# Kernel tuning notes

Measured on AMD Instinct MI355X. Metric: run time of the kernel, lower is better.

The kernel has to match this reference:

```python
import jax, jax.numpy as jnp
import numpy as np

N_CLUSTERS = 2048
MAX_ITER = 5


def setup_inputs() -> dict:
    key = jax.random.key(0)
    k1, k2 = jax.random.split(key)
    X = jax.random.normal(k1, (131072, 128), dtype=jnp.float32)
    init_centroids = jax.random.normal(k2, (N_CLUSTERS, 128), dtype=jnp.float32)
    return {"X": X, "init_centroids": init_centroids}


def _euc_sim(a, b):
    # 2 a.b^T - |a|^2 - |b|^2  (negative squared euclidean distance)
    return (2.0 * (a @ b.T)
            - jnp.sum(a * a, axis=1)[:, None]
            - jnp.sum(b * b, axis=1)[None, :])


def reference(X, init_centroids):
    K = init_centroids.shape[0]

    def step(centroids, _):
        sim = _euc_sim(X, centroids)              # [N, K]
        closest = jnp.argmax(sim, axis=-1)         # [N]
        sums = jax.ops.segment_sum(X, closest, num_segments=K)        # [K, d]
        counts = jax.ops.segment_sum(jnp.ones_like(closest, dtype=X.dtype),
                                     closest, num_segments=K)         # [K]
        # full-batch branch: c_grad = mask @ x / mask.sum(-1), NaN -> 0
        c_grad = jnp.where(counts[:, None] > 0, sums / jnp.maximum(counts, 1.0)[:, None], 0.0)
        # minibatch is None => lr = 1 => centroids <- c_grad
        return c_grad, closest

    centroids, closest_hist = jax.lax.scan(step, init_centroids, None, length=MAX_ITER)
    labels = closest_hist[-1]
    return centroids, labels
```

## Files before the change

### kernel.cpp

```cpp
#include <hip/hip_runtime.h>
#include <hip/hip_bf16.h>

#define NP 131072
#define D 128
#define KC 2048
#define ITERS 5
#define CG 8

#define TAU 0.03f
#define CNOFF 49152

#if defined(__has_builtin)
#if __has_builtin(__builtin_amdgcn_global_load_lds)
#define USE_GLL 1
#endif
#endif

typedef short bf16x8 __attribute__((ext_vector_type(8)));
typedef float f32x4 __attribute__((ext_vector_type(4)));

__device__ inline unsigned short f2bf(float x) {
    __hip_bfloat16 b = __float2bfloat16(x);
    return *reinterpret_cast<unsigned short*>(&b);
}
__device__ inline float bf2f(unsigned short u) {
    union { unsigned int i; float f; } c; c.i = ((unsigned int)u) << 16; return c.f;
}

__device__ inline size_t pslot(int k, int d, int hl) {
    int g = k >> 4, t15 = k & 15, ks = d >> 5, q = (d >> 3) & 3, e = d & 7;
    return ((size_t)((ks * 128 + g) * 2 + hl)) * 512 + (q * 16 + t15) * 8 + e;
}

#if USE_GLL
#define GLL16(srcp, dstp) __builtin_amdgcn_global_load_lds( \
    (const __attribute__((address_space(1))) unsigned int*)(srcp), \
    (__attribute__((address_space(3))) unsigned int*)(dstp), 16, 0, 0)
#define GLL4(srcp, dstp) __builtin_amdgcn_global_load_lds( \
    (const __attribute__((address_space(1))) unsigned int*)(srcp), \
    (__attribute__((address_space(3))) unsigned int*)(dstp), 4, 0, 0)
#else
#define GLL16(srcp, dstp) do { *(uint4*)((char*)(dstp) + lane * 16) = *(const uint4*)(srcp); } while (0)
#define GLL4(srcp, dstp)  do { *(unsigned int*)((char*)(dstp) + lane * 4) = *(const unsigned int*)(srcp); } while (0)
#endif

__global__ void init_kernel(const float* __restrict__ initC,
                            double* __restrict__ C64, double* __restrict__ CT64,
                            unsigned short* __restrict__ Pn) {
    int t = blockIdx.x * 256 + threadIdx.x;
    float v = initC[t];
    C64[t] = (double)v;
    CT64[(size_t)(t & 127) * KC + (t >> 7)] = (double)v;
    unsigned short h = f2bf(v);
    int k = t >> 7, d = t & 127;
    Pn[pslot(k, d, 0)] = h;
    Pn[pslot(k, d, 1)] = f2bf(v - bf2f(h));
}

__global__ void cnorm_kernel(const double* __restrict__ C64,
                             double* __restrict__ n64, float* __restrict__ n32,
                             int* __restrict__ counter) {
    int r = blockIdx.x * 4 + (threadIdx.x >> 6);
    int lane = threadIdx.x & 63;
    double a = C64[(size_t)r * D + lane * 2];
    double b = C64[(size_t)r * D + lane * 2 + 1];
    double s = a * a + b * b;
#pragma unroll
    for (int m = 1; m < 64; m <<= 1) s += __shfl_xor(s, m, 64);
    if (lane == 0) { n64[r] = s; n32[r] = (float)s; }
    if (blockIdx.x == 0 && threadIdx.x == 0) *counter = 0;
}

__global__ __launch_bounds__(256, 3)
void assign_kernel(const float* __restrict__ X,
                   const unsigned short* __restrict__ Pn,
                   const float* __restrict__ cnorm,
                   int* __restrict__ labels,
                   int* __restrict__ list,
                   int* __restrict__ counter) {
    __shared__ __align__(16) char lds[49664];

    const int tid = threadIdx.x;
    const int lane = tid & 63;
    const int wid = tid >> 6;
    const int wrow = wid >> 1;
    const int wcol = wid & 1;
    const int t15 = lane & 15;
    const int q = lane >> 4;
    const int pbase = blockIdx.x * 64;
    const char* PnB = (const char*)Pn;

#pragma unroll
    for (int i = 0; i < 8; i++) {
        int f = i * 256 + tid;
        int row = f >> 5, c4 = f & 31;
        float4 v = *(const float4*)&X[(size_t)(pbase + row) * D + c4 * 4];
        unsigned short h0 = f2bf(v.x), h1 = f2bf(v.y), h2 = f2bf(v.z), h3 = f2bf(v.w);
        unsigned short l0 = f2bf(v.x - bf2f(h0)), l1 = f2bf(v.y - bf2f(h1));
        unsigned short l2 = f2bf(v.z - bf2f(h2)), l3 = f2bf(v.w - bf2f(h3));
        uint2 ph = { (unsigned)h0 | ((unsigned)h1 << 16), (unsigned)h2 | ((unsigned)h3 << 16) };
        uint2 pl = { (unsigned)l0 | ((unsigned)l1 << 16), (unsigned)l2 | ((unsigned)l3 << 16) };
        int ad = (row * 256 + c4 * 8) ^ ((row & 7) << 4);
        *(uint2*)(lds + ad) = ph;
        *(uint2*)(lds + 16384 + ad) = pl;
    }
    __syncthreads();

    bf16x8 rah[2][4], ral[2][4];
#pragma unroll
    for (int rt = 0; rt < 2; rt++) {
        int row = wrow * 32 + rt * 16 + t15;
        int sw = (row & 7) << 4;
#pragma unroll
        for (int ks = 0; ks < 4; ks++) {
            int ad = (row * 256 + ks * 64 + q * 16) ^ sw;
            rah[rt][ks] = *(const bf16x8*)(lds + ad);
            ral[rt][ks] = *(const bf16x8*)(lds + 16384 + ad);
        }
    }
    __syncthreads();

    float b1[8], b2[8];
    int i1[8];
#pragma unroll
    for (int s = 0; s < 8; s++) { b1[s] = -INFINITY; b2[s] = -INFINITY; i1[s] = 0x7fffffff; }

#pragma unroll
    for (int i = 0; i < 4; i++) {
        int seg = wid * 4 + i;
        GLL16(PnB + seg * 1024 + lane * 16, lds + seg * 1024);
    }
#pragma unroll
    for (int i = 0; i < 4; i++) {
        int seg = wid * 4 + i;
        GLL16(PnB + (size_t)(1 * 128) * 2048 + seg * 1024 + lane * 16,
              lds + 16384 + seg * 1024);
    }

#define STEP(KS, VMSTR) do {                                                  \
        asm volatile("s_waitcnt vmcnt(" VMSTR ")" ::: "memory");              \
        __builtin_amdgcn_s_barrier();                                         \
        asm volatile("" ::: "memory");                                        \
        __builtin_amdgcn_sched_barrier(0);                                    \
        int t_ = ct * 4 + (KS);                                               \
        int s2_ = t_ + 2;                                                     \
        int s2c_ = (s2_ > 63) ? 63 : s2_;                                     \
        char* bstage_ = lds + (unsigned)(s2_ % 3) * 16384;                    \
        const char* nsrc_ = PnB + ((size_t)((s2c_ & 3) * 128 + (s2c_ >> 2) * 8)) * 2048; \
        _Pragma("unroll")                                                     \
        for (int i_ = 0; i_ < 4; i_++) {                                      \
            int seg_ = wid * 4 + i_;                                          \
            GLL16(nsrc_ + seg_ * 1024 + lane * 16, bstage_ + seg_ * 1024);    \
        }                                                                     \
        if ((KS) == 0) {                                                      \
            const float* cs_ = cnorm + ct * 128;                              \
            GLL4(cs_ + lane, lds + CNOFF);                                    \
            GLL4(cs_ + 64 + lane, lds + CNOFF + 256);                         \
        }                                                                     \
        const char* bcur_ = lds + (unsigned)(t_ % 3) * 16384;                 \
        __builtin_amdgcn_s_setprio(1);                                        \
        _Pragma("unroll")                                                     \
        for (int cj_ = 0; cj_ < 4; cj_++) {                                   \
            int gl_ = wcol * 4 + cj_;                                         \
            bf16x8 bh_ = *(const bf16x8*)(bcur_ + gl_ * 2048 + lane * 16);    \
            bf16x8 bl_ = *(const bf16x8*)(bcur_ + gl_ * 2048 + 1024 + lane * 16); \
            _Pragma("unroll")                                                 \
            for (int rt_ = 0; rt_ < 2; rt_++) {                               \
                acc[rt_][cj_] = __builtin_amdgcn_mfma_f32_16x16x32_bf16(rah[rt_][KS], bh_, acc[rt_][cj_], 0, 0, 0); \
                acc[rt_][cj_] = __builtin_amdgcn_mfma_f32_16x16x32_bf16(rah[rt_][KS], bl_, acc[rt_][cj_], 0, 0, 0); \
                acc[rt_][cj_] = __builtin_amdgcn_mfma_f32_16x16x32_bf16(ral[rt_][KS], bh_, acc[rt_][cj_], 0, 0, 0); \
            }                                                                 \
        }                                                                     \
        __builtin_amdgcn_s_setprio(0);                                        \
    } while (0)

    for (int ct = 0; ct < KC / 128; ct++) {
        f32x4 acc[2][4];
#pragma unroll
        for (int rt = 0; rt < 2; rt++)
#pragma unroll
            for (int cj = 0; cj < 4; cj++) acc[rt][cj] = (f32x4){0.f, 0.f, 0.f, 0.f};

        STEP(0, "4");
        STEP(1, "6");
        STEP(2, "6");
        STEP(3, "4");

        const float* cnL = (const float*)(lds + CNOFF);
#pragma unroll
        for (int cj = 0; cj < 4; cj++) {
            int col = ct * 128 + wcol * 64 + cj * 16 + t15;
            float cnv = cnL[wcol * 64 + cj * 16 + t15];
#pragma unroll
            for (int rt = 0; rt < 2; rt++)
#pragma unroll
                for (int rg = 0; rg < 4; rg++) {
                    int s = rt * 4 + rg;
                    float sv = __builtin_fmaf(2.0f, acc[rt][cj][rg], -cnv);
                    bool gt1 = sv > b1[s];
                    float mx2 = fmaxf(b2[s], sv);
                    b2[s] = gt1 ? b1[s] : mx2;
                    i1[s] = gt1 ? col : i1[s];
                    b1[s] = gt1 ? sv : b1[s];
                }
        }
    }
#undef STEP

#pragma unroll
    for (int s = 0; s < 8; s++) {
#pragma unroll
        for (int m = 1; m < 16; m <<= 1) {
            float ob1 = __shfl_xor(b1[s], m, 64);
            int   oi  = __shfl_xor(i1[s], m, 64);
            float ob2 = __shfl_xor(b2[s], m, 64);
            bool gt = ob1 > b1[s];
            bool eq = ob1 == b1[s];
            float nb2 = gt ? fmaxf(b1[s], ob2) : fmaxf(b2[s], ob1);
            nb2 = eq ? b1[s] : nb2;
            int ni = gt ? oi : i1[s];
            ni = (eq && oi < i1[s]) ? oi : ni;
            b1[s] = gt ? ob1 : b1[s];
            b2[s] = nb2;
            i1[s] = ni;
        }
    }

    __syncthreads();
    float* mb1 = (float*)lds;
    float* mb2 = ((float*)lds) + 128;
    int*   mi1 = (int*)(((float*)lds) + 256);
    if (t15 == 0) {
#pragma unroll
        for (int rt = 0; rt < 2; rt++)
#pragma unroll
            for (int rg = 0; rg < 4; rg++) {
                int s = rt * 4 + rg;
                int row = wrow * 32 + rt * 16 + q * 4 + rg;
                mb1[wcol * 64 + row] = b1[s];
                mb2[wcol * 64 + row] = b2[s];
                mi1[wcol * 64 + row] = i1[s];
            }
    }
    __syncthreads();
    if (tid < 64) {
        float a1 = mb1[tid], a2 = mb2[tid];  int ai = mi1[tid];
        float c1 = mb1[64 + tid], c2 = mb2[64 + tid];  int ci = mi1[64 + tid];
        float best, second;  int bi;
        if (a1 > c1)      { best = a1; bi = ai; second = fmaxf(a2, c1); }
        else if (a1 < c1) { best = c1; bi = ci; second = fmaxf(c2, a1); }
        else              { best = a1; bi = (ai < ci) ? ai : ci; second = a1; }
        int p = pbase + tid;
        labels[p] = bi;
        if (best - second < TAU) {
            int idx = atomicAdd(counter, 1);
            list[idx] = p;
        }
    }
}

__global__ void recheck_kernel(const float* __restrict__ X,
                               const double* __restrict__ CT64,
                               const double* __restrict__ cn64,
                               const int* __restrict__ list,
                               const int* __restrict__ counter,
                               int* __restrict__ labels) {
    __shared__ float xrow[D];
    __shared__ double rb[4];
    __shared__ int ri[4];
    int cnt = *counter;
    for (int ii = blockIdx.x; ii < cnt; ii += gridDim.x) {
        int p = list[ii];
        __syncthreads();
        if (threadIdx.x < D) xrow[threadIdx.x] = X[(size_t)p * D + threadIdx.x];
        __syncthreads();
        double xn = 0.0;
#pragma unroll 16
        for (int d = 0; d < D; d++) {
            double xv = (double)xrow[d];
            xn = fma(xv, xv, xn);
        }
        double best = -1.0e300;
        int bi = 0x7fffffff;
#pragma unroll
        for (int g = 0; g < 8; g++) {
            int c = threadIdx.x + 256 * g;
            double acc = 0.0;
#pragma unroll 16
            for (int d = 0; d < D; d++)
                acc = fma((double)xrow[d], CT64[(size_t)d * KC + c], acc);
            double s = 2.0 * acc - xn - cn64[c];
            if (s > best || (s == best && c < bi)) { best = s; bi = c; }
        }
#pragma unroll
        for (int m = 1; m < 64; m <<= 1) {
            double ob = __shfl_xor(best, m, 64);
            int oi = __shfl_xor(bi, m, 64);
            if (ob > best || (ob == best && oi < bi)) { best = ob; bi = oi; }
        }
        int w = threadIdx.x >> 6;
        if ((threadIdx.x & 63) == 0) { rb[w] = best; ri[w] = bi; }
        __syncthreads();
        if (threadIdx.x == 0) {
            double bb = rb[0]; int bbi = ri[0];
            for (int w2 = 1; w2 < 4; w2++)
                if (rb[w2] > bb || (rb[w2] == bb && ri[w2] < bbi)) { bb = rb[w2]; bbi = ri[w2]; }
            labels[p] = bbi;
        }
    }
}

__global__ __launch_bounds__(512)
void accum_kernel(const float* __restrict__ X,
                  const int* __restrict__ labels,
                  double* __restrict__ sums,
                  int* __restrict__ counts) {
    __shared__ double sred[8][CG][64][2];
    __shared__ int cred[8][CG];
    const int lane = threadIdx.x & 63;
    const int w = threadIdx.x >> 6;
    const int kbase = blockIdx.x * CG;
    const int base0 = w * (NP / 8);
    double s0[CG], s1[CG];
    int cnt[CG];
#pragma unroll
    for (int c = 0; c < CG; c++) { s0[c] = 0.0; s1[c] = 0.0; cnt[c] = 0; }

    for (int it = 0; it < (NP / 8) / 256; it++) {
        int4 lab = *(const int4*)&labels[base0 + it * 256 + lane * 4];
#pragma unroll
        for (int j = 0; j < 4; j++) {
            int lv = (j == 0) ? lab.x : (j == 1) ? lab.y : (j == 2) ? lab.z : lab.w;
            int rel = lv - kbase;
#pragma unroll
            for (int c = 0; c < CG; c++) {
                unsigned long long m = __ballot(rel == c);
                cnt[c] += __popcll(m);
                while (m) {
                    int b = __ffsll(m) - 1;
                    m &= m - 1;
                    int p = base0 + it * 256 + b * 4 + j;
                    float2 v = *(const float2*)&X[(size_t)p * D + lane * 2];
                    s0[c] += (double)v.x;
                    s1[c] += (double)v.y;
                }
            }
        }
    }
#pragma unroll
    for (int c = 0; c < CG; c++) {
        sred[w][c][lane][0] = s0[c];
        sred[w][c][lane][1] = s1[c];
    }
    if (lane < CG) cred[w][lane] = cnt[lane];
    __syncthreads();

#pragma unroll
    for (int rep = 0; rep < 2; rep++) {
        int idx = rep * 512 + threadIdx.x;
        int c = idx >> 7, d = idx & 127;
        double s = 0.0;
#pragma unroll
        for (int ww = 0; ww < 8; ww++) s += sred[ww][c][d >> 1][d & 1];
        sums[(size_t)(kbase + c) * D + d] = s;
    }
    if (threadIdx.x < CG) {
        int s = 0;
#pragma unroll
        for (int ww = 0; ww < 8; ww++) s += cred[ww][threadIdx.x];
        counts[kbase + threadIdx.x] = s;
    }
}

__global__ void update_kernel(const double* __restrict__ sums,
                              const int* __restrict__ counts,
                              double* __restrict__ C64, double* __restrict__ CT64,
                              unsigned short* __restrict__ Pn,
                              float* __restrict__ outC) {
    int t = blockIdx.x * 256 + threadIdx.x;
    int k = t >> 7;
    int n = counts[k];
    double v = (n > 0) ? sums[t] / (double)n : 0.0;
    C64[t] = v;
    CT64[(size_t)(t & 127) * KC + k] = v;
    float vf = (float)v;
    unsigned short h = f2bf(vf);
    int d = t & 127;
    Pn[pslot(k, d, 0)] = h;
    Pn[pslot(k, d, 1)] = f2bf(vf - bf2f(h));
    if (outC) outC[t] = vf;
}

__global__ void lab2f_kernel(const int* __restrict__ labels, float* __restrict__ out) {
    int t = blockIdx.x * 256 + threadIdx.x;
    out[t] = (float)labels[t];
}

extern "C" void kernel_launch(void* const* d_in, const int* in_sizes, int n_in,
                              void* d_out, int out_size, void* d_ws, size_t ws_size,
                              hipStream_t stream) {
    const float* X = (const float*)d_in[0];
    const float* initC = (const float*)d_in[1];
    float* out = (float*)d_out;

    char* w = (char*)d_ws;
    const size_t MB = 1u << 20;
    double* C64    = (double*)(w);
    double* S64    = (double*)(w + 2 * MB);
    double* CT64   = (double*)(w + 4 * MB);
    unsigned short* Pn = (unsigned short*)(w + 6 * MB);
    int*    labels = (int*)   (w + 7 * MB);
    int*    list   = (int*)   (w + 7 * MB + 512 * 1024);
    double* cn64   = (double*)(w + 8 * MB);
    float*  cn32   = (float*) (w + 8 * MB + 16 * 1024);
    int*    counts = (int*)   (w + 8 * MB + 24 * 1024);
    int*    counter= (int*)   (w + 8 * MB + 32 * 1024);

    init_kernel<<<(KC * D) / 256, 256, 0, stream>>>(initC, C64, CT64, Pn);

    for (int it = 0; it < ITERS; it++) {
        cnorm_kernel<<<KC / 4, 256, 0, stream>>>(C64, cn64, cn32, counter);
        assign_kernel<<<NP / 64, 256, 0, stream>>>(X, Pn, cn32, labels, list, counter);
        recheck_kernel<<<1024, 256, 0, stream>>>(X, CT64, cn64, list, counter, labels);
        accum_kernel<<<KC / CG, 512, 0, stream>>>(X, labels, S64, counts);
        update_kernel<<<(KC * D) / 256, 256, 0, stream>>>(
            S64, counts, C64, CT64, Pn, (it == ITERS - 1) ? out : nullptr);
    }
    lab2f_kernel<<<NP / 256, 256, 0, stream>>>(labels, out + (size_t)KC * D);
}
```

Before: 2.080 ms.

## Double assign tile to 128 points with 8 waves and fuse centroid norms into update

```diff
diff --git a/kernel.cpp b/kernel.cpp
--- a/kernel.cpp
+++ b/kernel.cpp
@@ -46,39 +46,38 @@
 
 __global__ void init_kernel(const float* __restrict__ initC,
                             double* __restrict__ C64, double* __restrict__ CT64,
-                            unsigned short* __restrict__ Pn) {
-    int t = blockIdx.x * 256 + threadIdx.x;
+                            unsigned short* __restrict__ Pn,
+                            double* __restrict__ cn64, float* __restrict__ cn32,
+                            int* __restrict__ counter) {
+    __shared__ double sred[4];
+    int tid = threadIdx.x;
+    int t = blockIdx.x * 256 + tid;
     float v = initC[t];
-    C64[t] = (double)v;
-    CT64[(size_t)(t & 127) * KC + (t >> 7)] = (double)v;
+    double dv = (double)v;
+    C64[t] = dv;
+    CT64[(size_t)(t & 127) * KC + (t >> 7)] = dv;
     unsigned short h = f2bf(v);
     int k = t >> 7, d = t & 127;
     Pn[pslot(k, d, 0)] = h;
     Pn[pslot(k, d, 1)] = f2bf(v - bf2f(h));
-}
-
-__global__ void cnorm_kernel(const double* __restrict__ C64,
-                             double* __restrict__ n64, float* __restrict__ n32,
-                             int* __restrict__ counter) {
-    int r = blockIdx.x * 4 + (threadIdx.x >> 6);
-    int lane = threadIdx.x & 63;
-    double a = C64[(size_t)r * D + lane * 2];
-    double b = C64[(size_t)r * D + lane * 2 + 1];
-    double s = a * a + b * b;
+    double s = dv * dv;
 #pragma unroll
     for (int m = 1; m < 64; m <<= 1) s += __shfl_xor(s, m, 64);
-    if (lane == 0) { n64[r] = s; n32[r] = (float)s; }
-    if (blockIdx.x == 0 && threadIdx.x == 0) *counter = 0;
-}
-
-__global__ __launch_bounds__(256, 3)
+    if ((tid & 63) == 0) sred[tid >> 6] = s;
+    __syncthreads();
+    if (tid == 0)   { double ss = sred[0] + sred[1]; cn64[k] = ss; cn32[k] = (float)ss; }
+    if (tid == 128) { double ss = sred[2] + sred[3]; cn64[k] = ss; cn32[k] = (float)ss; }
+    if (blockIdx.x == 0 && tid == 0) *counter = 0;
+}
+
+__global__ __launch_bounds__(512, 2)
 void assign_kernel(const float* __restrict__ X,
                    const unsigned short* __restrict__ Pn,
                    const float* __restrict__ cnorm,
                    int* __restrict__ labels,
                    int* __restrict__ list,
                    int* __restrict__ counter) {
-    __shared__ __align__(16) char lds[49664];
+    __shared__ __align__(16) char lds[65536];
 
     const int tid = threadIdx.x;
     const int lane = tid & 63;
@@ -87,12 +86,12 @@
     const int wcol = wid & 1;
     const int t15 = lane & 15;
     const int q = lane >> 4;
-    const int pbase = blockIdx.x * 64;
+    const int pbase = blockIdx.x * 128;
     const char* PnB = (const char*)Pn;
 
 #pragma unroll
     for (int i = 0; i < 8; i++) {
-        int f = i * 256 + tid;
+        int f = i * 512 + tid;
         int row = f >> 5, c4 = f & 31;
         float4 v = *(const float4*)&X[(size_t)(pbase + row) * D + c4 * 4];
         unsigned short h0 = f2bf(v.x), h1 = f2bf(v.y), h2 = f2bf(v.z), h3 = f2bf(v.w);
@@ -102,7 +101,7 @@
         uint2 pl = { (unsigned)l0 | ((unsigned)l1 << 16), (unsigned)l2 | ((unsigned)l3 << 16) };
         int ad = (row * 256 + c4 * 8) ^ ((row & 7) << 4);
         *(uint2*)(lds + ad) = ph;
-        *(uint2*)(lds + 16384 + ad) = pl;
+        *(uint2*)(lds + 32768 + ad) = pl;
     }
     __syncthreads();
 
@@ -115,7 +114,7 @@
         for (int ks = 0; ks < 4; ks++) {
             int ad = (row * 256 + ks * 64 + q * 16) ^ sw;
             rah[rt][ks] = *(const bf16x8*)(lds + ad);
-            ral[rt][ks] = *(const bf16x8*)(lds + 16384 + ad);
+            ral[rt][ks] = *(const bf16x8*)(lds + 32768 + ad);
         }
     }
     __syncthreads();
@@ -126,14 +125,14 @@
     for (int s = 0; s < 8; s++) { b1[s] = -INFINITY; b2[s] = -INFINITY; i1[s] = 0x7fffffff; }
 
 #pragma unroll
-    for (int i = 0; i < 4; i++) {
-        int seg = wid * 4 + i;
+    for (int i = 0; i < 2; i++) {
+        int seg = wid * 2 + i;
         GLL16(PnB + seg * 1024 + lane * 16, lds + seg * 1024);
     }
 #pragma unroll
-    for (int i = 0; i < 4; i++) {
-        int seg = wid * 4 + i;
-        GLL16(PnB + (size_t)(1 * 128) * 2048 + seg * 1024 + lane * 16,
+    for (int i = 0; i < 2; i++) {
+        int seg = wid * 2 + i;
+        GLL16(PnB + (size_t)128 * 2048 + seg * 1024 + lane * 16,
               lds + 16384 + seg * 1024);
     }
 
@@ -148,8 +147,8 @@
         char* bstage_ = lds + (unsigned)(s2_ % 3) * 16384;                    \
         const char* nsrc_ = PnB + ((size_t)((s2c_ & 3) * 128 + (s2c_ >> 2) * 8)) * 2048; \
         _Pragma("unroll")                                                     \
-        for (int i_ = 0; i_ < 4; i_++) {                                      \
-            int seg_ = wid * 4 + i_;                                          \
+        for (int i_ = 0; i_ < 2; i_++) {                                      \
+            int seg_ = wid * 2 + i_;                                          \
             GLL16(nsrc_ + seg_ * 1024 + lane * 16, bstage_ + seg_ * 1024);    \
         }                                                                     \
         if ((KS) == 0) {                                                      \
@@ -181,10 +180,10 @@
 #pragma unroll
             for (int cj = 0; cj < 4; cj++) acc[rt][cj] = (f32x4){0.f, 0.f, 0.f, 0.f};
 
-        STEP(0, "4");
-        STEP(1, "6");
-        STEP(2, "6");
-        STEP(3, "4");
+        STEP(0, "2");
+        STEP(1, "4");
+        STEP(2, "4");
+        STEP(3, "2");
 
         const float* cnL = (const float*)(lds + CNOFF);
 #pragma unroll
@@ -228,8 +227,8 @@
 
     __syncthreads();
     float* mb1 = (float*)lds;
-    float* mb2 = ((float*)lds) + 128;
-    int*   mi1 = (int*)(((float*)lds) + 256);
+    float* mb2 = ((float*)lds) + 256;
+    int*   mi1 = (int*)(((float*)lds) + 512);
     if (t15 == 0) {
 #pragma unroll
         for (int rt = 0; rt < 2; rt++)
@@ -237,15 +236,15 @@
             for (int rg = 0; rg < 4; rg++) {
                 int s = rt * 4 + rg;
                 int row = wrow * 32 + rt * 16 + q * 4 + rg;
-                mb1[wcol * 64 + row] = b1[s];
-                mb2[wcol * 64 + row] = b2[s];
-                mi1[wcol * 64 + row] = i1[s];
+                mb1[wcol * 128 + row] = b1[s];
+                mb2[wcol * 128 + row] = b2[s];
+                mi1[wcol * 128 + row] = i1[s];
             }
     }
     __syncthreads();
-    if (tid < 64) {
+    if (tid < 128) {
         float a1 = mb1[tid], a2 = mb2[tid];  int ai = mi1[tid];
-        float c1 = mb1[64 + tid], c2 = mb2[64 + tid];  int ci = mi1[64 + tid];
+        float c1 = mb1[128 + tid], c2 = mb2[128 + tid];  int ci = mi1[128 + tid];
         float best, second;  int bi;
         if (a1 > c1)      { best = a1; bi = ai; second = fmaxf(a2, c1); }
         else if (a1 < c1) { best = c1; bi = ci; second = fmaxf(c2, a1); }
@@ -376,8 +375,12 @@
                               const int* __restrict__ counts,
                               double* __restrict__ C64, double* __restrict__ CT64,
                               unsigned short* __restrict__ Pn,
+                              double* __restrict__ cn64, float* __restrict__ cn32,
+                              int* __restrict__ counter,
                               float* __restrict__ outC) {
-    int t = blockIdx.x * 256 + threadIdx.x;
+    __shared__ double sred[4];
+    int tid = threadIdx.x;
+    int t = blockIdx.x * 256 + tid;
     int k = t >> 7;
     int n = counts[k];
     double v = (n > 0) ? sums[t] / (double)n : 0.0;
@@ -389,6 +392,14 @@
     Pn[pslot(k, d, 0)] = h;
     Pn[pslot(k, d, 1)] = f2bf(vf - bf2f(h));
     if (outC) outC[t] = vf;
+    double s = v * v;
+#pragma unroll
+    for (int m = 1; m < 64; m <<= 1) s += __shfl_xor(s, m, 64);
+    if ((tid & 63) == 0) sred[tid >> 6] = s;
+    __syncthreads();
+    if (tid == 0)   { double ss = sred[0] + sred[1]; cn64[k] = ss; cn32[k] = (float)ss; }
+    if (tid == 128) { double ss = sred[2] + sred[3]; cn64[k] = ss; cn32[k] = (float)ss; }
+    if (blockIdx.x == 0 && tid == 0) *counter = 0;
 }
 
 __global__ void lab2f_kernel(const int* __restrict__ labels, float* __restrict__ out) {
@@ -416,15 +427,15 @@
     int*    counts = (int*)   (w + 8 * MB + 24 * 1024);
     int*    counter= (int*)   (w + 8 * MB + 32 * 1024);
 
-    init_kernel<<<(KC * D) / 256, 256, 0, stream>>>(initC, C64, CT64, Pn);
+    init_kernel<<<(KC * D) / 256, 256, 0, stream>>>(initC, C64, CT64, Pn, cn64, cn32, counter);
 
     for (int it = 0; it < ITERS; it++) {
-        cnorm_kernel<<<KC / 4, 256, 0, stream>>>(C64, cn64, cn32, counter);
-        assign_kernel<<<NP / 64, 256, 0, stream>>>(X, Pn, cn32, labels, list, counter);
+        assign_kernel<<<NP / 128, 512, 0, stream>>>(X, Pn, cn32, labels, list, counter);
         recheck_kernel<<<1024, 256, 0, stream>>>(X, CT64, cn64, list, counter, labels);
         accum_kernel<<<KC / CG, 512, 0, stream>>>(X, labels, S64, counts);
         update_kernel<<<(KC * D) / 256, 256, 0, stream>>>(
-            S64, counts, C64, CT64, Pn, (it == ITERS - 1) ? out : nullptr);
+            S64, counts, C64, CT64, Pn, cn64, cn32, counter,
+            (it == ITERS - 1) ? out : nullptr);
     }
     lab2f_kernel<<<NP / 256, 256, 0, stream>>>(labels, out + (size_t)KC * D);
 }
```

Result: slower. 2.189 ms (+5.3%).

## Batch 8 points per recheck block and fuse centroid norms into init/update

Applied to the files above, without the earlier changes.

```diff
diff --git a/kernel.cpp b/kernel.cpp
--- a/kernel.cpp
+++ b/kernel.cpp
@@ -46,29 +46,28 @@
 
 __global__ void init_kernel(const float* __restrict__ initC,
                             double* __restrict__ C64, double* __restrict__ CT64,
-                            unsigned short* __restrict__ Pn) {
-    int t = blockIdx.x * 256 + threadIdx.x;
+                            unsigned short* __restrict__ Pn,
+                            double* __restrict__ cn64, float* __restrict__ cn32,
+                            int* __restrict__ counter) {
+    __shared__ double sred[4];
+    int tid = threadIdx.x;
+    int t = blockIdx.x * 256 + tid;
     float v = initC[t];
-    C64[t] = (double)v;
-    CT64[(size_t)(t & 127) * KC + (t >> 7)] = (double)v;
+    double dv = (double)v;
+    C64[t] = dv;
+    CT64[(size_t)(t & 127) * KC + (t >> 7)] = dv;
     unsigned short h = f2bf(v);
     int k = t >> 7, d = t & 127;
     Pn[pslot(k, d, 0)] = h;
     Pn[pslot(k, d, 1)] = f2bf(v - bf2f(h));
-}
-
-__global__ void cnorm_kernel(const double* __restrict__ C64,
-                             double* __restrict__ n64, float* __restrict__ n32,
-                             int* __restrict__ counter) {
-    int r = blockIdx.x * 4 + (threadIdx.x >> 6);
-    int lane = threadIdx.x & 63;
-    double a = C64[(size_t)r * D + lane * 2];
-    double b = C64[(size_t)r * D + lane * 2 + 1];
-    double s = a * a + b * b;
+    double s = dv * dv;
 #pragma unroll
     for (int m = 1; m < 64; m <<= 1) s += __shfl_xor(s, m, 64);
-    if (lane == 0) { n64[r] = s; n32[r] = (float)s; }
-    if (blockIdx.x == 0 && threadIdx.x == 0) *counter = 0;
+    if ((tid & 63) == 0) sred[tid >> 6] = s;
+    __syncthreads();
+    if (tid == 0)   { double ss = sred[0] + sred[1]; cn64[k] = ss; cn32[k] = (float)ss; }
+    if (tid == 128) { double ss = sred[2] + sred[3]; cn64[k] = ss; cn32[k] = (float)ss; }
+    if (blockIdx.x == 0 && tid == 0) *counter = 0;
 }
 
 __global__ __launch_bounds__(256, 3)
@@ -259,53 +258,90 @@
     }
 }
 
-__global__ void recheck_kernel(const float* __restrict__ X,
-                               const double* __restrict__ CT64,
-                               const double* __restrict__ cn64,
-                               const int* __restrict__ list,
-                               const int* __restrict__ counter,
-                               int* __restrict__ labels) {
-    __shared__ float xrow[D];
-    __shared__ double rb[4];
-    __shared__ int ri[4];
+__global__ __launch_bounds__(256)
+void recheck_kernel(const float* __restrict__ X,
+                    const double* __restrict__ CT64,
+                    const double* __restrict__ cn64,
+                    const int* __restrict__ list,
+                    const int* __restrict__ counter,
+                    int* __restrict__ labels) {
+    __shared__ float xrow[8][D];
+    __shared__ double xnS[8];
+    __shared__ double rb[4][8];
+    __shared__ int ri[4][8];
     int cnt = *counter;
-    for (int ii = blockIdx.x; ii < cnt; ii += gridDim.x) {
-        int p = list[ii];
+    for (int base = blockIdx.x * 8; base < cnt; base += gridDim.x * 8) {
+        int np8 = (cnt - base < 8) ? (cnt - base) : 8;
         __syncthreads();
-        if (threadIdx.x < D) xrow[threadIdx.x] = X[(size_t)p * D + threadIdx.x];
+#pragma unroll
+        for (int j = 0; j < 4; j++) {
+            int idx = j * 256 + threadIdx.x;
+            int r = idx >> 7, d = idx & 127;
+            if (r < np8) {
+                int p = list[base + r];
+                xrow[r][d] = X[(size_t)p * D + d];
+            }
+        }
         __syncthreads();
-        double xn = 0.0;
-#pragma unroll 16
-        for (int d = 0; d < D; d++) {
-            double xv = (double)xrow[d];
-            xn = fma(xv, xv, xn);
-        }
-        double best = -1.0e300;
-        int bi = 0x7fffffff;
-#pragma unroll
+        if (threadIdx.x < 8) {
+            double xn = 0.0;
+            if (threadIdx.x < np8) {
+                for (int d = 0; d < D; d++) {
+                    double xv = (double)xrow[threadIdx.x][d];
+                    xn = fma(xv, xv, xn);
+                }
+            }
+            xnS[threadIdx.x] = xn;
+        }
+        __syncthreads();
+
+        double best[8];
+        int bi[8];
+#pragma unroll
+        for (int p = 0; p < 8; p++) { best[p] = -1.0e300; bi[p] = 0x7fffffff; }
+
         for (int g = 0; g < 8; g++) {
             int c = threadIdx.x + 256 * g;
-            double acc = 0.0;
-#pragma unroll 16
-            for (int d = 0; d < D; d++)
-                acc = fma((double)xrow[d], CT64[(size_t)d * KC + c], acc);
-            double s = 2.0 * acc - xn - cn64[c];
-            if (s > best || (s == best && c < bi)) { best = s; bi = c; }
-        }
-#pragma unroll
-        for (int m = 1; m < 64; m <<= 1) {
-            double ob = __shfl_xor(best, m, 64);
-            int oi = __shfl_xor(bi, m, 64);
-            if (ob > best || (ob == best && oi < bi)) { best = ob; bi = oi; }
-        }
-        int w = threadIdx.x >> 6;
-        if ((threadIdx.x & 63) == 0) { rb[w] = best; ri[w] = bi; }
+            double acc[8];
+#pragma unroll
+            for (int p = 0; p < 8; p++) acc[p] = 0.0;
+#pragma unroll 8
+            for (int d = 0; d < D; d++) {
+                double wv = CT64[(size_t)d * KC + c];
+#pragma unroll
+                for (int p = 0; p < 8; p++)
+                    acc[p] = fma((double)xrow[p][d], wv, acc[p]);
+            }
+            double cn = cn64[c];
+#pragma unroll
+            for (int p = 0; p < 8; p++) {
+                double s = 2.0 * acc[p] - xnS[p] - cn;
+                if (s > best[p] || (s == best[p] && c < bi[p])) { best[p] = s; bi[p] = c; }
+            }
+        }
+
+#pragma unroll
+        for (int p = 0; p < 8; p++) {
+#pragma unroll
+            for (int m = 1; m < 64; m <<= 1) {
+                double ob = __shfl_xor(best[p], m, 64);
+                int oi = __shfl_xor(bi[p], m, 64);
+                if (ob > best[p] || (ob == best[p] && oi < bi[p])) { best[p] = ob; bi[p] = oi; }
+            }
+        }
+        int wv2 = threadIdx.x >> 6;
+        if ((threadIdx.x & 63) == 0) {
+#pragma unroll
+            for (int p = 0; p < 8; p++) { rb[wv2][p] = best[p]; ri[wv2][p] = bi[p]; }
+        }
         __syncthreads();
-        if (threadIdx.x == 0) {
-            double bb = rb[0]; int bbi = ri[0];
+        if (threadIdx.x < np8) {
+            int p = threadIdx.x;
+            double bb = rb[0][p]; int bbi = ri[0][p];
+#pragma unroll
             for (int w2 = 1; w2 < 4; w2++)
-                if (rb[w2] > bb || (rb[w2] == bb && ri[w2] < bbi)) { bb = rb[w2]; bbi = ri[w2]; }
-            labels[p] = bbi;
+                if (rb[w2][p] > bb || (rb[w2][p] == bb && ri[w2][p] < bbi)) { bb = rb[w2][p]; bbi = ri[w2][p]; }
+            labels[list[base + p]] = bbi;
         }
     }
 }
@@ -376,8 +412,12 @@
                               const int* __restrict__ counts,
                               double* __restrict__ C64, double* __restrict__ CT64,
                               unsigned short* __restrict__ Pn,
+                              double* __restrict__ cn64, float* __restrict__ cn32,
+                              int* __restrict__ counter,
                               float* __restrict__ outC) {
-    int t = blockIdx.x * 256 + threadIdx.x;
+    __shared__ double sred[4];
+    int tid = threadIdx.x;
+    int t = blockIdx.x * 256 + tid;
     int k = t >> 7;
     int n = counts[k];
     double v = (n > 0) ? sums[t] / (double)n : 0.0;
@@ -389,6 +429,14 @@
     Pn[pslot(k, d, 0)] = h;
     Pn[pslot(k, d, 1)] = f2bf(vf - bf2f(h));
     if (outC) outC[t] = vf;
+    double s = v * v;
+#pragma unroll
+    for (int m = 1; m < 64; m <<= 1) s += __shfl_xor(s, m, 64);
+    if ((tid & 63) == 0) sred[tid >> 6] = s;
+    __syncthreads();
+    if (tid == 0)   { double ss = sred[0] + sred[1]; cn64[k] = ss; cn32[k] = (float)ss; }
+    if (tid == 128) { double ss = sred[2] + sred[3]; cn64[k] = ss; cn32[k] = (float)ss; }
+    if (blockIdx.x == 0 && tid == 0) *counter = 0;
 }
 
 __global__ void lab2f_kernel(const int* __restrict__ labels, float* __restrict__ out) {
@@ -416,15 +464,15 @@
     int*    counts = (int*)   (w + 8 * MB + 24 * 1024);
     int*    counter= (int*)   (w + 8 * MB + 32 * 1024);
 
-    init_kernel<<<(KC * D) / 256, 256, 0, stream>>>(initC, C64, CT64, Pn);
+    init_kernel<<<(KC * D) / 256, 256, 0, stream>>>(initC, C64, CT64, Pn, cn64, cn32, counter);
 
     for (int it = 0; it < ITERS; it++) {
-        cnorm_kernel<<<KC / 4, 256, 0, stream>>>(C64, cn64, cn32, counter);
         assign_kernel<<<NP / 64, 256, 0, stream>>>(X, Pn, cn32, labels, list, counter);
-        recheck_kernel<<<1024, 256, 0, stream>>>(X, CT64, cn64, list, counter, labels);
+        recheck_kernel<<<256, 256, 0, stream>>>(X, CT64, cn64, list, counter, labels);
         accum_kernel<<<KC / CG, 512, 0, stream>>>(X, labels, S64, counts);
         update_kernel<<<(KC * D) / 256, 256, 0, stream>>>(
-            S64, counts, C64, CT64, Pn, (it == ITERS - 1) ? out : nullptr);
+            S64, counts, C64, CT64, Pn, cn64, cn32, counter,
+            (it == ITERS - 1) ? out : nullptr);
     }
     lab2f_kernel<<<NP / 256, 256, 0, stream>>>(labels, out + (size_t)KC * D);
 }
```

New measurement: 2.907 ms. 1.4x slower.

## Fuse centroid update and norm computation into accum and init kernels

Applied to the files above, without the earlier changes.

```diff
diff --git a/kernel.cpp b/kernel.cpp
--- a/kernel.cpp
+++ b/kernel.cpp
@@ -7,7 +7,7 @@
 #define ITERS 5
 #define CG 8
 
-#define TAU 0.03f
+#define TAU 0.015f
 #define CNOFF 49152
 
 #if defined(__has_builtin)
@@ -46,29 +46,28 @@
 
 __global__ void init_kernel(const float* __restrict__ initC,
                             double* __restrict__ C64, double* __restrict__ CT64,
-                            unsigned short* __restrict__ Pn) {
-    int t = blockIdx.x * 256 + threadIdx.x;
+                            unsigned short* __restrict__ Pn,
+                            double* __restrict__ cn64, float* __restrict__ cn32,
+                            int* __restrict__ counter) {
+    __shared__ double sred[4];
+    int tid = threadIdx.x;
+    int t = blockIdx.x * 256 + tid;
     float v = initC[t];
-    C64[t] = (double)v;
-    CT64[(size_t)(t & 127) * KC + (t >> 7)] = (double)v;
+    double dv = (double)v;
+    C64[t] = dv;
+    CT64[(size_t)(t & 127) * KC + (t >> 7)] = dv;
     unsigned short h = f2bf(v);
     int k = t >> 7, d = t & 127;
     Pn[pslot(k, d, 0)] = h;
     Pn[pslot(k, d, 1)] = f2bf(v - bf2f(h));
-}
-
-__global__ void cnorm_kernel(const double* __restrict__ C64,
-                             double* __restrict__ n64, float* __restrict__ n32,
-                             int* __restrict__ counter) {
-    int r = blockIdx.x * 4 + (threadIdx.x >> 6);
-    int lane = threadIdx.x & 63;
-    double a = C64[(size_t)r * D + lane * 2];
-    double b = C64[(size_t)r * D + lane * 2 + 1];
-    double s = a * a + b * b;
+    double s = dv * dv;
 #pragma unroll
     for (int m = 1; m < 64; m <<= 1) s += __shfl_xor(s, m, 64);
-    if (lane == 0) { n64[r] = s; n32[r] = (float)s; }
-    if (blockIdx.x == 0 && threadIdx.x == 0) *counter = 0;
+    if ((tid & 63) == 0) sred[tid >> 6] = s;
+    __syncthreads();
+    if (tid == 0)   { double ss = sred[0] + sred[1]; cn64[k] = ss; cn32[k] = (float)ss; }
+    if (tid == 128) { double ss = sred[2] + sred[3]; cn64[k] = ss; cn32[k] = (float)ss; }
+    if (blockIdx.x == 0 && tid == 0) *counter = 0;
 }
 
 __global__ __launch_bounds__(256, 3)
@@ -313,10 +312,15 @@
 __global__ __launch_bounds__(512)
 void accum_kernel(const float* __restrict__ X,
                   const int* __restrict__ labels,
-                  double* __restrict__ sums,
-                  int* __restrict__ counts) {
+                  double* __restrict__ C64, double* __restrict__ CT64,
+                  unsigned short* __restrict__ Pn,
+                  double* __restrict__ cn64, float* __restrict__ cn32,
+                  int* __restrict__ counter,
+                  float* __restrict__ outC) {
     __shared__ double sred[8][CG][64][2];
     __shared__ int cred[8][CG];
+    __shared__ int cntS[CG];
+    __shared__ double cnp[2][8];
     const int lane = threadIdx.x & 63;
     const int w = threadIdx.x >> 6;
     const int kbase = blockIdx.x * CG;
@@ -355,6 +359,14 @@
     if (lane < CG) cred[w][lane] = cnt[lane];
     __syncthreads();
 
+    if (threadIdx.x < CG) {
+        int s = 0;
+#pragma unroll
+        for (int ww = 0; ww < 8; ww++) s += cred[ww][threadIdx.x];
+        cntS[threadIdx.x] = s;
+    }
+    __syncthreads();
+
 #pragma unroll
     for (int rep = 0; rep < 2; rep++) {
         int idx = rep * 512 + threadIdx.x;
@@ -362,33 +374,30 @@
         double s = 0.0;
 #pragma unroll
         for (int ww = 0; ww < 8; ww++) s += sred[ww][c][d >> 1][d & 1];
-        sums[(size_t)(kbase + c) * D + d] = s;
-    }
+        int k = kbase + c;
+        int n = cntS[c];
+        double v = (n > 0) ? s / (double)n : 0.0;
+        C64[(size_t)k * D + d] = v;
+        CT64[(size_t)d * KC + k] = v;
+        float vf = (float)v;
+        unsigned short h = f2bf(vf);
+        Pn[pslot(k, d, 0)] = h;
+        Pn[pslot(k, d, 1)] = f2bf(vf - bf2f(h));
+        if (outC) outC[(size_t)k * D + d] = vf;
+        double sq = v * v;
+#pragma unroll
+        for (int m = 1; m < 64; m <<= 1) sq += __shfl_xor(sq, m, 64);
+        if (lane == 0) cnp[rep][w] = sq;
+    }
+    __syncthreads();
     if (threadIdx.x < CG) {
-        int s = 0;
-#pragma unroll
-        for (int ww = 0; ww < 8; ww++) s += cred[ww][threadIdx.x];
-        counts[kbase + threadIdx.x] = s;
-    }
-}
-
-__global__ void update_kernel(const double* __restrict__ sums,
-                              const int* __restrict__ counts,
-                              double* __restrict__ C64, double* __restrict__ CT64,
-                              unsigned short* __restrict__ Pn,
-                              float* __restrict__ outC) {
-    int t = blockIdx.x * 256 + threadIdx.x;
-    int k = t >> 7;
-    int n = counts[k];
-    double v = (n > 0) ? sums[t] / (double)n : 0.0;
-    C64[t] = v;
-    CT64[(size_t)(t & 127) * KC + k] = v;
-    float vf = (float)v;
-    unsigned short h = f2bf(vf);
-    int d = t & 127;
-    Pn[pslot(k, d, 0)] = h;
-    Pn[pslot(k, d, 1)] = f2bf(vf - bf2f(h));
-    if (outC) outC[t] = vf;
+        int c = threadIdx.x;
+        int rep = c >> 2, wp = (c & 3) * 2;
+        double cn = cnp[rep][wp] + cnp[rep][wp + 1];
+        cn64[kbase + c] = cn;
+        cn32[kbase + c] = (float)cn;
+    }
+    if (blockIdx.x == 0 && threadIdx.x == 0) *counter = 0;
 }
 
 __global__ void lab2f_kernel(const int* __restrict__ labels, float* __restrict__ out) {
@@ -406,25 +415,21 @@
     char* w = (char*)d_ws;
     const size_t MB = 1u << 20;
     double* C64    = (double*)(w);
-    double* S64    = (double*)(w + 2 * MB);
     double* CT64   = (double*)(w + 4 * MB);
     unsigned short* Pn = (unsigned short*)(w + 6 * MB);
     int*    labels = (int*)   (w + 7 * MB);
     int*    list   = (int*)   (w + 7 * MB + 512 * 1024);
     double* cn64   = (double*)(w + 8 * MB);
     float*  cn32   = (float*) (w + 8 * MB + 16 * 1024);
-    int*    counts = (int*)   (w + 8 * MB + 24 * 1024);
     int*    counter= (int*)   (w + 8 * MB + 32 * 1024);
 
-    init_kernel<<<(KC * D) / 256, 256, 0, stream>>>(initC, C64, CT64, Pn);
+    init_kernel<<<(KC * D) / 256, 256, 0, stream>>>(initC, C64, CT64, Pn, cn64, cn32, counter);
 
     for (int it = 0; it < ITERS; it++) {
-        cnorm_kernel<<<KC / 4, 256, 0, stream>>>(C64, cn64, cn32, counter);
         assign_kernel<<<NP / 64, 256, 0, stream>>>(X, Pn, cn32, labels, list, counter);
-        recheck_kernel<<<1024, 256, 0, stream>>>(X, CT64, cn64, list, counter, labels);
-        accum_kernel<<<KC / CG, 512, 0, stream>>>(X, labels, S64, counts);
-        update_kernel<<<(KC * D) / 256, 256, 0, stream>>>(
-            S64, counts, C64, CT64, Pn, (it == ITERS - 1) ? out : nullptr);
+        recheck_kernel<<<2048, 256, 0, stream>>>(X, CT64, cn64, list, counter, labels);
+        accum_kernel<<<KC / CG, 512, 0, stream>>>(X, labels, C64, CT64, Pn, cn64, cn32,
+                                                  counter, (it == ITERS - 1) ? out : nullptr);
     }
     lab2f_kernel<<<NP / 256, 256, 0, stream>>>(labels, out + (size_t)KC * D);
 }
```

Result: faster. 1.845 ms (-11.3%).
